# Performance work log

Measured on AMD Instinct MI355X. Metric: run time of the kernel, lower is better.

The kernel has to match this reference:

```python
import jax, jax.numpy as jnp
import numpy as np

N = 50000      # nodes
E = 800000     # edges (avg degree 16)
F_IN = 128     # num_node_features
H = 128        # hidden_dim
G = 500        # num graphs in batch


def setup_inputs() -> dict:
    key = jax.random.key(0)
    ks = jax.random.split(key, 20)
    inp = {
        "x": jax.random.normal(ks[0], (N, F_IN), dtype=jnp.float32),
        "edge_index": jax.random.randint(ks[1], (2, E), 0, N, dtype=jnp.int32),
        "batch": jnp.sort(jax.random.randint(ks[2], (N,), 0, G, dtype=jnp.int32)),
    }
    s = 0.05
    # 3 GIN layers: MLP = Linear -> ReLU -> Linear, plus learnable eps (init 0)
    dims = [(F_IN, H), (H, H), (H, H)]
    for i, (din, dout) in enumerate(dims):
        k = jax.random.split(ks[3 + i], 4)
        inp[f"W1_{i}"] = jax.random.normal(k[0], (din, H), dtype=jnp.float32) * s
        inp[f"b1_{i}"] = jnp.zeros((H,), dtype=jnp.float32)
        inp[f"W2_{i}"] = jax.random.normal(k[1], (H, dout), dtype=jnp.float32) * s
        inp[f"b2_{i}"] = jnp.zeros((dout,), dtype=jnp.float32)
        inp[f"eps_{i}"] = jnp.zeros((), dtype=jnp.float32)
    inp["fc_w"] = jax.random.normal(ks[10], (H, 1), dtype=jnp.float32) * s
    inp["fc_b"] = jnp.zeros((1,), dtype=jnp.float32)
    return inp


def _gin_layer(x, src, dst, eps, W1, b1, W2, b2):
    # neighbor sum: scatter-add messages x[src] into dst rows
    agg = jax.ops.segment_sum(x[src], dst, num_segments=N)  # [N, d]
    h = (1.0 + eps) * x + agg
    h = jax.nn.relu(h @ W1 + b1) @ W2 + b2
    return h


def reference(x, edge_index, batch,
              W1_0, b1_0, W2_0, b2_0, eps_0,
              W1_1, b1_1, W2_1, b2_1, eps_1,
              W1_2, b1_2, W2_2, b2_2, eps_2,
              fc_w, fc_b):
    src, dst = edge_index[0], edge_index[1]
    layers = [(eps_0, W1_0, b1_0, W2_0, b2_0),
              (eps_1, W1_1, b1_1, W2_1, b2_1),
              (eps_2, W1_2, b1_2, W2_2, b2_2)]
    h = x
    for i, (eps, W1, b1, W2, b2) in enumerate(layers):
        h = _gin_layer(h, src, dst, eps, W1, b1, W2, b2)
        if i < len(layers) - 1:
            h = jax.nn.relu(h)  # dropout is identity in eval mode
    # global mean pool over graph ids
    sums = jax.ops.segment_sum(h, batch, num_segments=G)          # [G, H]
    counts = jax.ops.segment_sum(jnp.ones((N,), h.dtype), batch, num_segments=G)
    pooled = sums / jnp.maximum(counts, 1.0)[:, None]
    out = pooled @ fc_w + fc_b  # [G, 1]
    return jnp.squeeze(out, axis=-1)  # [G]
```

## Files before the change

### kernel.cpp

```cpp
#include <hip/hip_runtime.h>


#define FEAT 128
#define BCAP 2048

typedef short  bf16x8 __attribute__((ext_vector_type(8)));
typedef float  f32x4  __attribute__((ext_vector_type(4)));

__device__ inline unsigned short f2bf(float f) {
    unsigned int u = __float_as_uint(f);
    u = (u + 0x7FFFu + ((u >> 16) & 1u)) >> 16;
    return (unsigned short)u;
}
__device__ inline float2 bfpair(unsigned int u) {
    float2 r;
    r.x = __uint_as_float(u << 16);
    r.y = __uint_as_float(u & 0xffff0000u);
    return r;
}

__global__ void bucket_kernel(const int* __restrict__ src, const int* __restrict__ dst,
                              int* __restrict__ bcnt, unsigned int* __restrict__ bpairs,
                              int E) {
    int e = blockIdx.x * blockDim.x + threadIdx.x;
    if (e >= E) return;
    int d = dst[e], s = src[e];
    int cb = d >> 6;
    int p = atomicAdd(&bcnt[cb * 16], 1);
    if (p < BCAP) bpairs[(size_t)cb * BCAP + p] = ((unsigned int)s << 6) | (unsigned int)(d & 63);
}

__global__ __launch_bounds__(256) void deg_kernel(const int* __restrict__ bcnt,
                                                  const unsigned int* __restrict__ bpairs,
                                                  int* __restrict__ off, int n) {
    __shared__ int lh[64];
    int b = blockIdx.x, tid = threadIdx.x;
    if (tid < 64) lh[tid] = 0;
    __syncthreads();
    int cnt = bcnt[b * 16]; if (cnt > BCAP) cnt = BCAP;
    const unsigned int* bp = bpairs + (size_t)b * BCAP;
    for (int i = tid; i < cnt; i += 256) atomicAdd(&lh[bp[i] & 63u], 1);
    __syncthreads();
    if (tid < 64) {
        int node = b * 64 + tid;
        if (node < n) off[node] = lh[tid];
    }
}

__global__ void block_sum_kernel(const int* __restrict__ off, int* __restrict__ bs, int n) {
    int b = blockIdx.x, t = threadIdx.x;
    int base = b * 1024;
    int s = 0;
    #pragma unroll
    for (int i = 0; i < 4; ++i) {
        int idx = base + t + 256 * i;
        if (idx < n) s += off[idx];
    }
    #pragma unroll
    for (int d = 32; d; d >>= 1) s += __shfl_down(s, d, 64);
    __shared__ int ws[4];
    if ((t & 63) == 0) ws[t >> 6] = s;
    __syncthreads();
    if (t == 0) bs[b] = ws[0] + ws[1] + ws[2] + ws[3];
}

__global__ void scan_blocksums_kernel(int* __restrict__ bs, int nb,
                                      int* __restrict__ off, int n) {
    __shared__ int l[1024];
    int t = threadIdx.x;
    int v = (t < nb) ? bs[t] : 0;
    l[t] = v;
    __syncthreads();
    for (int d = 1; d < 1024; d <<= 1) {
        int u = (t >= d) ? l[t - d] : 0;
        __syncthreads();
        l[t] += u;
        __syncthreads();
    }
    if (t < nb) bs[t] = (t == 0) ? 0 : l[t - 1];
    if (t == 1023) off[n] = l[1023];
}

__global__ __launch_bounds__(256) void block_scan_kernel(
    int* __restrict__ off, const int* __restrict__ bs, int n) {
    __shared__ int l[1024];
    __shared__ int part[256];
    int b = blockIdx.x, t = threadIdx.x;
    int base = b * 1024;
    #pragma unroll
    for (int i = 0; i < 4; ++i) {
        int idx = base + t + 256 * i;
        l[t + 256 * i] = (idx < n) ? off[idx] : 0;
    }
    __syncthreads();
    int v0 = l[4 * t], v1 = l[4 * t + 1], v2 = l[4 * t + 2], v3 = l[4 * t + 3];
    int p = v0 + v1 + v2 + v3;
    part[t] = p;
    __syncthreads();
    for (int d = 1; d < 256; d <<= 1) {
        int u = (t >= d) ? part[t - d] : 0;
        __syncthreads();
        part[t] += u;
        __syncthreads();
    }
    int ex = bs[b] + ((t == 0) ? 0 : part[t - 1]);
    int e0 = ex, e1 = ex + v0, e2 = e1 + v1, e3 = e2 + v2;
    int idx = base + 4 * t;
    if (idx + 3 < n) {
        ((int4*)(off + idx))[0] = make_int4(e0, e1, e2, e3);
    } else {
        if (idx + 0 < n) off[idx + 0] = e0;
        if (idx + 1 < n) off[idx + 1] = e1;
        if (idx + 2 < n) off[idx + 2] = e2;
    }
}

__global__ __launch_bounds__(256) void bucket_scatter_kernel(
    const int* __restrict__ bcnt, const unsigned int* __restrict__ bpairs,
    const int* __restrict__ off, int* __restrict__ srcs, int n) {
    __shared__ int lcur[64];
    int b = blockIdx.x, tid = threadIdx.x;
    if (tid < 64) {
        int node = b * 64 + tid;
        lcur[tid] = (node < n) ? off[node] : 0;
    }
    __syncthreads();
    int cnt = bcnt[b * 16]; if (cnt > BCAP) cnt = BCAP;
    const unsigned int* bp = bpairs + (size_t)b * BCAP;
    for (int i = tid; i < cnt; i += 256) {
        unsigned int pr = bp[i];
        int pos = atomicAdd(&lcur[pr & 63u], 1);
        srcs[pos] = (int)(pr >> 6);
    }
}

__global__ __launch_bounds__(256) void setup_kernel(
    const float* __restrict__ x, unsigned int* __restrict__ xbf, long pairs, int nxb,
    const int* __restrict__ batch, int* __restrict__ gstart, int n, int G,
    const float* __restrict__ W2f, const float* __restrict__ b2f,
    const float* __restrict__ fcw, float* __restrict__ weff,
    const float* __restrict__ W0, const float* __restrict__ W1,
    const float* __restrict__ W2, const float* __restrict__ W3,
    const float* __restrict__ W4, unsigned short* __restrict__ Wswz) {
    int b = blockIdx.x, tid = threadIdx.x;
    if (b < nxb) {
        long i = (long)b * 256 + tid;
        if (i < pairs) {
            float2 v = ((const float2*)x)[i];
            xbf[i] = (unsigned int)f2bf(v.x) | ((unsigned int)f2bf(v.y) << 16);
        }
    } else if (b < nxb + 2) {
        int i = (b - nxb) * 256 + tid;
        if (i <= G) {
            int lo = 0, hi = n;
            while (lo < hi) { int m = (lo + hi) >> 1; if (batch[m] < i) lo = m + 1; else hi = m; }
            gstart[i] = lo;
        }
    } else if (b == nxb + 2) {
        int lane = tid & 63, wave = tid >> 6;
        float2 f2 = ((const float2*)fcw)[lane];
        for (int r = wave; r < 128; r += 4) {
            float2 w = ((const float2*)(W2f + r * FEAT))[lane];
            float d = w.x * f2.x + w.y * f2.y;
            #pragma unroll
            for (int s = 32; s; s >>= 1) d += __shfl_down(d, s, 64);
            if (lane == 0) weff[r] = d;
        }
        if (wave == 0) {
            float2 bb = ((const float2*)b2f)[lane];
            float d = bb.x * f2.x + bb.y * f2.y;
            #pragma unroll
            for (int s = 32; s; s >>= 1) d += __shfl_down(d, s, 64);
            if (lane == 0) weff[128] = d;
        }
    } else {
        int gid = (b - nxb - 3) * 256 + tid;
        if (gid < 5 * 2048) {
            int mat = gid >> 11;
            int task = gid & 2047;
            int c = task >> 4, m = task & 15;
            const float* W = (mat == 0) ? W0 : (mat == 1) ? W1 : (mat == 2) ? W2 :
                             (mat == 3) ? W3 : W4;
            unsigned short* dp = Wswz + mat * 16384 + c * 128 + ((m ^ (c & 7)) << 3);
            #pragma unroll
            for (int j = 0; j < 8; ++j) dp[j] = f2bf(W[(8 * m + j) * FEAT + c]);
        }
    }
}

__global__ void agg_kernel(const unsigned int* __restrict__ h, const int* __restrict__ off,
                           const int* __restrict__ srcs, const float* __restrict__ eps_p,
                           unsigned int* __restrict__ pre_bf, int n) {
    int wave = (int)((blockIdx.x * (size_t)blockDim.x + threadIdx.x) >> 6);
    int lane = threadIdx.x & 63;
    if (wave >= n) return;
    float eps1 = 1.0f + eps_p[0];
    float2 self = bfpair(h[(size_t)wave * 64 + lane]);
    float2 acc0 = make_float2(self.x * eps1, self.y * eps1);
    float2 acc1 = make_float2(0.f, 0.f);
    float2 acc2 = make_float2(0.f, 0.f);
    float2 acc3 = make_float2(0.f, 0.f);
    int j0 = off[wave], j1 = off[wave + 1];
    int j = j0;
    for (; j + 8 <= j1; j += 8) {
        int s0 = srcs[j + 0], s1 = srcs[j + 1], s2 = srcs[j + 2], s3 = srcs[j + 3];
        int s4 = srcs[j + 4], s5 = srcs[j + 5], s6 = srcs[j + 6], s7 = srcs[j + 7];
        unsigned int u0 = h[(size_t)s0 * 64 + lane];
        unsigned int u1 = h[(size_t)s1 * 64 + lane];
        unsigned int u2 = h[(size_t)s2 * 64 + lane];
        unsigned int u3 = h[(size_t)s3 * 64 + lane];
        unsigned int u4 = h[(size_t)s4 * 64 + lane];
        unsigned int u5 = h[(size_t)s5 * 64 + lane];
        unsigned int u6 = h[(size_t)s6 * 64 + lane];
        unsigned int u7 = h[(size_t)s7 * 64 + lane];
        float2 v0 = bfpair(u0), v1 = bfpair(u1), v2 = bfpair(u2), v3 = bfpair(u3);
        float2 v4 = bfpair(u4), v5 = bfpair(u5), v6 = bfpair(u6), v7 = bfpair(u7);
        acc0.x += v0.x; acc0.y += v0.y;  acc1.x += v1.x; acc1.y += v1.y;
        acc2.x += v2.x; acc2.y += v2.y;  acc3.x += v3.x; acc3.y += v3.y;
        acc0.x += v4.x; acc0.y += v4.y;  acc1.x += v5.x; acc1.y += v5.y;
        acc2.x += v6.x; acc2.y += v6.y;  acc3.x += v7.x; acc3.y += v7.y;
    }
    for (; j < j1; ++j) {
        int s = srcs[j];
        float2 v = bfpair(h[(size_t)s * 64 + lane]);
        acc0.x += v.x; acc0.y += v.y;
    }
    acc0.x += acc1.x + acc2.x + acc3.x;
    acc0.y += acc1.y + acc2.y + acc3.y;
    pre_bf[(size_t)wave * 64 + lane] =
        (unsigned int)f2bf(acc0.x) | ((unsigned int)f2bf(acc0.y) << 16);
}

template <int MODE>
__global__ __launch_bounds__(256) void mfma_mlp_kernel(
    const unsigned short* __restrict__ A, const unsigned short* __restrict__ Wswz,
    const float* __restrict__ bias, unsigned short* __restrict__ outbf,
    const int* __restrict__ batch, const float* __restrict__ weff,
    float* __restrict__ sums, int n) {
    __shared__ int4 Wl4[2048];
    int tid = threadIdx.x;
    const int4* ws4 = (const int4*)Wswz;
    #pragma unroll
    for (int i = 0; i < 8; ++i) Wl4[i * 256 + tid] = ws4[i * 256 + tid];
    __syncthreads();
    const unsigned short* Wl = (const unsigned short*)Wl4;

    int lane = tid & 63, wave = tid >> 6;
    int q = lane >> 4, c15 = lane & 15;
    int r0 = blockIdx.x * 64 + wave * 16;
    int arow = r0 + c15;
    bool rv = arow < n;
    const bf16x8* ap = (const bf16x8*)(A + (size_t)arow * FEAT + q * 8);

    f32x4 zf = {0.f, 0.f, 0.f, 0.f};
    f32x4 acc[8];
    #pragma unroll
    for (int i = 0; i < 8; ++i) acc[i] = zf;
    bf16x8 zero8 = {0, 0, 0, 0, 0, 0, 0, 0};

    #pragma unroll
    for (int k0 = 0; k0 < 4; ++k0) {
        bf16x8 a = rv ? ap[k0 * 4] : zero8;
        int m = k0 * 4 + q;
        #pragma unroll
        for (int nt = 0; nt < 8; ++nt) {
            int col = nt * 16 + c15;
            bf16x8 b = *(const bf16x8*)&Wl[col * 128 + ((m ^ (col & 7)) << 3)];
            acc[nt] = __builtin_amdgcn_mfma_f32_16x16x32_bf16(a, b, acc[nt], 0, 0, 0);
        }
    }

    int orow0 = r0 + q * 4;
    if (MODE == 1) {
        #pragma unroll
        for (int nt = 0; nt < 8; ++nt) {
            int col = nt * 16 + c15;
            float bv = bias[col];
            #pragma unroll
            for (int r = 0; r < 4; ++r) {
                int ro = orow0 + r;
                if (ro < n) {
                    float v = fmaxf(acc[nt][r] + bv, 0.f);
                    outbf[(size_t)ro * FEAT + col] = f2bf(v);
                }
            }
        }
    } else {
        __shared__ float gsum[64];
        int r0b = blockIdx.x * 64;
        int lastn = r0b + 63 < n - 1 ? r0b + 63 : n - 1;
        int gmin = batch[r0b];
        int gmax = batch[lastn];
        int span = gmax - gmin + 1;
        bool lds_ok = (span <= 64);
        if (lds_ok) for (int i = tid; i < span; i += 256) gsum[i] = 0.f;
        __syncthreads();
        float rowdot[4] = {0.f, 0.f, 0.f, 0.f};
        #pragma unroll
        for (int nt = 0; nt < 8; ++nt) {
            int col = nt * 16 + c15;
            float bv = bias[col];
            float wv = weff[col];
            #pragma unroll
            for (int r = 0; r < 4; ++r)
                rowdot[r] += fmaxf(acc[nt][r] + bv, 0.f) * wv;
        }
        #pragma unroll
        for (int r = 0; r < 4; ++r) {
            float v = rowdot[r];
            v += __shfl_xor(v, 1, 64);
            v += __shfl_xor(v, 2, 64);
            v += __shfl_xor(v, 4, 64);
            v += __shfl_xor(v, 8, 64);
            if (c15 == 0) {
                int node = orow0 + r;
                if (node < n) {
                    int g = batch[node];
                    if (lds_ok) atomicAdd(&gsum[g - gmin], v);
                    else        atomicAdd(&sums[g], v);
                }
            }
        }
        __syncthreads();
        if (lds_ok)
            for (int i = tid; i < span; i += 256) atomicAdd(&sums[gmin + i], gsum[i]);
    }
}

__global__ void finalize_kernel(const float* __restrict__ sums, const int* __restrict__ gstart,
                                const float* __restrict__ weff, const float* __restrict__ fcb,
                                float* __restrict__ out, int G) {
    int g = blockIdx.x * blockDim.x + threadIdx.x;
    if (g >= G) return;
    int cnt = gstart[g + 1] - gstart[g];
    out[g] = (cnt > 0) ? sums[g] / (float)cnt + weff[128] + fcb[0] : fcb[0];
}

static inline size_t align256(size_t x) { return (x + 255) & ~(size_t)255; }

extern "C" void kernel_launch(void* const* d_in, const int* in_sizes, int n_in,
                              void* d_out, int out_size, void* d_ws, size_t ws_size,
                              hipStream_t stream) {
    const float* x      = (const float*)d_in[0];
    const int*   ei     = (const int*)d_in[1];
    const int*   batch  = (const int*)d_in[2];
    const float* W1[3]  = {(const float*)d_in[3],  (const float*)d_in[8],  (const float*)d_in[13]};
    const float* b1[3]  = {(const float*)d_in[4],  (const float*)d_in[9],  (const float*)d_in[14]};
    const float* W2[3]  = {(const float*)d_in[5],  (const float*)d_in[10], (const float*)d_in[15]};
    const float* b2[3]  = {(const float*)d_in[6],  (const float*)d_in[11], (const float*)d_in[16]};
    const float* eps[3] = {(const float*)d_in[7],  (const float*)d_in[12], (const float*)d_in[17]};
    const float* fcw    = (const float*)d_in[18];
    const float* fcb    = (const float*)d_in[19];
    float* out = (float*)d_out;

    const int N = in_sizes[0] / FEAT;
    const int E = in_sizes[1] / 2;
    const int G = out_size;
    const int nbuckets = (N + 63) >> 6;

    char* p = (char*)d_ws;
    int* off    = (int*)p;  p += align256((size_t)(N + 1) * 4);
    int* srcs   = (int*)p;  p += align256((size_t)E * 4);
    int* bsums  = (int*)p;  p += align256((size_t)1024 * 4);
    int* gstart = (int*)p;  p += align256((size_t)(G + 1) * 4);
    float* weff = (float*)p; p += align256((size_t)256 * 4);
    unsigned short* Wswz = (unsigned short*)p; p += align256((size_t)5 * 16384 * 2);
    float* sums = (float*)p;
    char* z0 = (char*)sums;
    p += align256((size_t)G * 4);
    int* bcnt = (int*)p; p += align256((size_t)nbuckets * 16 * 4);
    size_t zbytes = (size_t)(p - z0);
    unsigned int* bpairs = (unsigned int*)p;     p += align256((size_t)nbuckets * BCAP * 4);
    unsigned int* x_bf   = (unsigned int*)p;     p += align256((size_t)N * 64 * 4);
    unsigned int* pre_bf = (unsigned int*)p;     p += align256((size_t)N * 64 * 4);
    unsigned int* t_bf   = (unsigned int*)p;     p += align256((size_t)N * 64 * 4);
    unsigned int* h_bf   = (unsigned int*)p;     p += align256((size_t)N * 64 * 4);
    (void)ws_size; (void)n_in;

    const int* src = ei;
    const int* dst = ei + E;

    hipMemsetAsync(z0, 0, zbytes, stream);

    const int nb = (N + 1023) / 1024;
    bucket_kernel<<<(E + 255) / 256, 256, 0, stream>>>(src, dst, bcnt, bpairs, E);
    deg_kernel<<<nbuckets, 256, 0, stream>>>(bcnt, bpairs, off, N);
    block_sum_kernel<<<nb, 256, 0, stream>>>(off, bsums, N);
    scan_blocksums_kernel<<<1, 1024, 0, stream>>>(bsums, nb, off, N);
    block_scan_kernel<<<nb, 256, 0, stream>>>(off, bsums, N);
    bucket_scatter_kernel<<<nbuckets, 256, 0, stream>>>(bcnt, bpairs, off, srcs, N);

    long pairs = (long)N * 64;
    int nxb = (int)((pairs + 255) / 256);
    setup_kernel<<<nxb + 43, 256, 0, stream>>>(
        x, x_bf, pairs, nxb, batch, gstart, N, G,
        W2[2], b2[2], fcw, weff,
        W1[0], W2[0], W1[1], W2[1], W1[2], Wswz);

    const int aggBlocks  = (N + 3) / 4;
    const int gemmBlocks = (N + 63) / 64;
    const unsigned short* Wz[5] = {Wswz, Wswz + 16384, Wswz + 2 * 16384,
                                   Wswz + 3 * 16384, Wswz + 4 * 16384};

    const unsigned int* h = x_bf;
    for (int i = 0; i < 2; ++i) {
        agg_kernel<<<aggBlocks, 256, 0, stream>>>(h, off, srcs, eps[i], pre_bf, N);
        mfma_mlp_kernel<1><<<gemmBlocks, 256, 0, stream>>>(
            (const unsigned short*)pre_bf, Wz[2 * i], b1[i], (unsigned short*)t_bf,
            nullptr, nullptr, nullptr, N);
        mfma_mlp_kernel<1><<<gemmBlocks, 256, 0, stream>>>(
            (const unsigned short*)t_bf, Wz[2 * i + 1], b2[i], (unsigned short*)h_bf,
            nullptr, nullptr, nullptr, N);
        h = h_bf;
    }
    agg_kernel<<<aggBlocks, 256, 0, stream>>>(h, off, srcs, eps[2], pre_bf, N);
    mfma_mlp_kernel<2><<<gemmBlocks, 256, 0, stream>>>(
        (const unsigned short*)pre_bf, Wz[4], b1[2], nullptr,
        batch, weff, sums, N);

    finalize_kernel<<<(G + 255) / 256, 256, 0, stream>>>(sums, gstart, weff, fcb, out, G);
}
```

Measured before the change: 350.4 us.

## Replace per-edge global atomics in bucketing with block-local counting sort

The edge-bucketing kernel now gives each block a chunk of 10240 edges. It counts destination buckets in shared memory, prefix-scans those counts, and reserves space with one global atomic per bucket per block. Edges are then staged in LDS in bucket order and written out as contiguous runs, using a binary search over the bucket bases to find each edge's slot. This removes heavy contention from roughly a thousand atomics landing on each global counter, and makes the output writes more coalesced. In exchange, the grid shrinks to about 79 blocks, far fewer than the GPU has compute units, and each block pays extra scan and search work.

```diff
diff --git a/kernel.cpp b/kernel.cpp
--- a/kernel.cpp
+++ b/kernel.cpp
@@ -3,6 +3,7 @@
 
 #define FEAT 128
 #define BCAP 2048
+#define CHUNK 10240
 
 typedef short  bf16x8 __attribute__((ext_vector_type(8)));
 typedef float  f32x4  __attribute__((ext_vector_type(4)));
@@ -19,15 +20,59 @@
     return r;
 }
 
-__global__ void bucket_kernel(const int* __restrict__ src, const int* __restrict__ dst,
-                              int* __restrict__ bcnt, unsigned int* __restrict__ bpairs,
-                              int E) {
-    int e = blockIdx.x * blockDim.x + threadIdx.x;
-    if (e >= E) return;
-    int d = dst[e], s = src[e];
-    int cb = d >> 6;
-    int p = atomicAdd(&bcnt[cb * 16], 1);
-    if (p < BCAP) bpairs[(size_t)cb * BCAP + p] = ((unsigned int)s << 6) | (unsigned int)(d & 63);
+__global__ __launch_bounds__(256) void bucket_kernel(
+    const int* __restrict__ src, const int* __restrict__ dst,
+    int* __restrict__ bcnt, unsigned int* __restrict__ bpairs, int E) {
+    __shared__ unsigned int lpairs[CHUNK];
+    __shared__ int lbase[1025];
+    __shared__ int lcur[1024];
+    __shared__ int lres[1024];
+    __shared__ int part[256];
+    int tid = threadIdx.x;
+    int e0 = blockIdx.x * CHUNK;
+    int e1 = e0 + CHUNK; if (e1 > E) e1 = E;
+    int cnt = e1 - e0;
+    #pragma unroll
+    for (int i = 0; i < 4; ++i) lcur[tid + 256 * i] = 0;
+    __syncthreads();
+    for (int e = e0 + tid; e < e1; e += 256) atomicAdd(&lcur[dst[e] >> 6], 1);
+    __syncthreads();
+    int v0 = lcur[4 * tid], v1 = lcur[4 * tid + 1], v2 = lcur[4 * tid + 2], v3 = lcur[4 * tid + 3];
+    part[tid] = v0 + v1 + v2 + v3;
+    __syncthreads();
+    for (int d = 1; d < 256; d <<= 1) {
+        int u = (tid >= d) ? part[tid - d] : 0;
+        __syncthreads();
+        part[tid] += u;
+        __syncthreads();
+    }
+    int ex = (tid == 0) ? 0 : part[tid - 1];
+    lbase[4 * tid] = ex;
+    lbase[4 * tid + 1] = ex + v0;
+    lbase[4 * tid + 2] = ex + v0 + v1;
+    lbase[4 * tid + 3] = ex + v0 + v1 + v2;
+    if (tid == 255) lbase[1024] = part[255];
+    __syncthreads();
+    #pragma unroll
+    for (int i = 0; i < 4; ++i) {
+        int b = tid + 256 * i;
+        lcur[b] = lbase[b];
+        int c = lbase[b + 1] - lbase[b];
+        lres[b] = (c > 0) ? atomicAdd(&bcnt[b * 16], c) : 0;
+    }
+    __syncthreads();
+    for (int e = e0 + tid; e < e1; e += 256) {
+        int d = dst[e], s = src[e];
+        int p = atomicAdd(&lcur[d >> 6], 1);
+        lpairs[p] = ((unsigned int)s << 6) | (unsigned int)(d & 63);
+    }
+    __syncthreads();
+    for (int j = tid; j < cnt; j += 256) {
+        int lo = 0, hi = 1023;
+        while (lo < hi) { int m = (lo + hi + 1) >> 1; if (lbase[m] <= j) lo = m; else hi = m - 1; }
+        int gpos = lres[lo] + (j - lbase[lo]);
+        if (gpos < BCAP) bpairs[(size_t)lo * BCAP + gpos] = lpairs[j];
+    }
 }
 
 __global__ __launch_bounds__(256) void deg_kernel(const int* __restrict__ bcnt,
@@ -383,7 +428,8 @@
     hipMemsetAsync(z0, 0, zbytes, stream);
 
     const int nb = (N + 1023) / 1024;
-    bucket_kernel<<<(E + 255) / 256, 256, 0, stream>>>(src, dst, bcnt, bpairs, E);
+    const int nchunks = (E + CHUNK - 1) / CHUNK;
+    bucket_kernel<<<nchunks, 256, 0, stream>>>(src, dst, bcnt, bpairs, E);
     deg_kernel<<<nbuckets, 256, 0, stream>>>(bcnt, bpairs, off, N);
     block_sum_kernel<<<nb, 256, 0, stream>>>(off, bsums, N);
     scan_blocksums_kernel<<<1, 1024, 0, stream>>>(bsums, nb, off, N);
```

Measured after the change: 361.9 us. +3.3%, slower.
